# Kernel optimization log

Hardware: AMD Instinct MI355X
Metric: run time of the kernel (lower is better)

Reference implementation:

```python
import jax, jax.numpy as jnp
import numpy as np
import math

DIM = 1536; NH = 12; HD = 128
F, H, W = 6, 30, 30
S = F * H * W
B = 1
K_LEN = 9900  # hardcoded k_lens in the source forward
EPS_NORM = 1e-6


def _rope_tables(max_len=1024, d=HD):
    # Wan rope_params: three tables of widths d-4*(d//6), 2*(d//6), 2*(d//6)
    # -> cos/sin tables of half-widths 22, 21, 21 (concat = d//2 = 64)
    def ang(dd):
        inv = 1.0 / (10000.0 ** (np.arange(0, dd, 2, dtype=np.float64) / dd))
        return np.outer(np.arange(max_len, dtype=np.float64), inv)
    a = np.concatenate([ang(d - 4 * (d // 6)), ang(2 * (d // 6)), ang(2 * (d // 6))], axis=1)
    return np.cos(a).astype(np.float32), np.sin(a).astype(np.float32)


def setup_inputs() -> dict:
    key = jax.random.key(0)
    ks = jax.random.split(key, 5)
    s = 1.0 / math.sqrt(DIM)
    cos, sin = _rope_tables()
    return {
        "x": jax.random.normal(ks[0], (B, S, DIM), jnp.float32),
        "q_w": jax.random.normal(ks[1], (DIM, DIM), jnp.float32) * s,
        "q_b": jnp.zeros((DIM,), jnp.float32),
        "k_w": jax.random.normal(ks[2], (DIM, DIM), jnp.float32) * s,
        "k_b": jnp.zeros((DIM,), jnp.float32),
        "v_w": jax.random.normal(ks[3], (DIM, DIM), jnp.float32) * s,
        "v_b": jnp.zeros((DIM,), jnp.float32),
        "o_w": jax.random.normal(ks[4], (DIM, DIM), jnp.float32) * s,
        "o_b": jnp.zeros((DIM,), jnp.float32),
        "norm_q_w": jnp.ones((DIM,), jnp.float32),
        "norm_k_w": jnp.ones((DIM,), jnp.float32),
        "freqs_cos": jnp.asarray(cos),
        "freqs_sin": jnp.asarray(sin),
        "grid_f": F, "grid_h": H, "grid_w": W,
    }


def rms_norm(x, w):
    # RMSNorm over full model dim, computed in fp32 (as in source)
    xf = x.astype(jnp.float32)
    xn = xf * jax.lax.rsqrt(jnp.mean(xf * xf, axis=-1, keepdims=True) + EPS_NORM)
    return xn.astype(x.dtype) * w


def rope_apply(x, cos, sin, f, h, w):
    # x: [B,S,N,D]; rotate consecutive pairs with 3D-factorized (f,h,w) freqs
    Bb, Ss, Nn, Dd = x.shape
    c = Dd // 2
    sp = [c - 2 * (c // 3), c // 3, c // 3]  # 22, 21, 21

    def grid(tab):
        tf = tab[:, :sp[0]]
        th = tab[:, sp[0]:sp[0] + sp[1]]
        tw = tab[:, sp[0] + sp[1]:]
        g = jnp.concatenate([
            jnp.broadcast_to(tf[:f, None, None, :], (f, h, w, sp[0])),
            jnp.broadcast_to(th[None, :h, None, :], (f, h, w, sp[1])),
            jnp.broadcast_to(tw[None, None, :w, :], (f, h, w, sp[2])),
        ], axis=-1)
        return g.reshape(f * h * w, 1, c)  # [S,1,c] (broadcast over heads)

    gc, gs = grid(cos), grid(sin)
    xp = x.astype(jnp.float32).reshape(Bb, Ss, Nn, c, 2)
    xr, xi = xp[..., 0], xp[..., 1]
    orr = xr * gc - xi * gs
    oii = xr * gs + xi * gc
    return jnp.stack([orr, oii], axis=-1).reshape(Bb, Ss, Nn, Dd).astype(x.dtype)


def attention(q, k, v, k_len):
    # full attention (window_size=(-1,-1)) with keys masked beyond k_len
    scale = 1.0 / math.sqrt(q.shape[-1])
    att = jnp.einsum('bqnd,bknd->bnqk', q, k) * scale
    valid = jnp.arange(k.shape[1]) < k_len
    att = jnp.where(valid[None, None, None, :], att, jnp.finfo(att.dtype).min)
    p = jax.nn.softmax(att, axis=-1)
    return jnp.einsum('bnqk,bknd->bqnd', p, v)


def reference(x, q_w, q_b, k_w, k_b, v_w, v_b, o_w, o_b, norm_q_w, norm_k_w, freqs_cos, freqs_sin, grid_f, grid_h, grid_w):
    Bb, Ss, _ = x.shape
    q = rms_norm(x @ q_w.T + q_b, norm_q_w).reshape(Bb, Ss, NH, HD)
    k = rms_norm(x @ k_w.T + k_b, norm_k_w).reshape(Bb, Ss, NH, HD)
    v = (x @ v_w.T + v_b).reshape(Bb, Ss, NH, HD)
    q = rope_apply(q, freqs_cos, freqs_sin, grid_f, grid_h, grid_w)
    k = rope_apply(k, freqs_cos, freqs_sin, grid_f, grid_h, grid_w)
    o = attention(q, k, v, K_LEN).reshape(Bb, Ss, NH * HD)
    return o @ o_w.T + o_b
```

## Files before the change

kernel.cpp:

```cpp
#include <hip/hip_runtime.h>

#define DIM 1536
#define NH 12
#define HD 128
#define S_LEN 5400
#define SPAD 5440
#define MPAD 5504
#define NQKV 4608
#define EPS_NORM 1e-6f

typedef __bf16 bf16_t;
typedef __bf16 bf16x8 __attribute__((ext_vector_type(8)));
typedef __bf16 bf16x4 __attribute__((ext_vector_type(4)));
typedef float  f32x4  __attribute__((ext_vector_type(4)));

#define GLOAD_LDS16(gp, lp) __builtin_amdgcn_global_load_lds( \
    (__attribute__((address_space(1))) void*)(void*)(gp),     \
    (__attribute__((address_space(3))) void*)(lp), 16, 0, 0)


__global__ __launch_bounds__(256) void cvt_x_kernel(const float* __restrict__ x,
                                                    bf16_t* __restrict__ xb) {
  size_t base = ((size_t)blockIdx.x * 256 + threadIdx.x) * 4;
  if (base >= (size_t)MPAD * DIM) return;
  size_t row = base / DIM;
  float4 v = make_float4(0.f, 0.f, 0.f, 0.f);
  if (row < S_LEN) v = *(const float4*)&x[base];
  bf16x4 o; o[0] = (__bf16)v.x; o[1] = (__bf16)v.y; o[2] = (__bf16)v.z; o[3] = (__bf16)v.w;
  *(bf16x4*)&xb[base] = o;
}

__global__ __launch_bounds__(256) void cvt_wqkv_kernel(const float* __restrict__ qw,
                                                       const float* __restrict__ kw,
                                                       const float* __restrict__ vw,
                                                       bf16_t* __restrict__ wb) {
  size_t base = ((size_t)blockIdx.x * 256 + threadIdx.x) * 4;
  if (base >= (size_t)NQKV * DIM) return;
  int row = (int)(base / DIM);
  int col = (int)(base - (size_t)row * DIM);
  const float* src; int rr = row;
  if (rr >= 3072)      { src = vw; rr -= 3072; }
  else if (rr >= 1536) { src = kw; rr -= 1536; }
  else                 { src = qw; }
  float4 v = *(const float4*)&src[(size_t)rr * DIM + col];
  bf16x4 o; o[0] = (__bf16)v.x; o[1] = (__bf16)v.y; o[2] = (__bf16)v.z; o[3] = (__bf16)v.w;
  *(bf16x4*)&wb[base] = o;
}

__global__ __launch_bounds__(256) void cvt_wo_kernel(const float* __restrict__ w,
                                                     bf16_t* __restrict__ wb) {
  size_t base = ((size_t)blockIdx.x * 256 + threadIdx.x) * 4;
  if (base >= (size_t)DIM * DIM) return;
  float4 v = *(const float4*)&w[base];
  bf16x4 o; o[0] = (__bf16)v.x; o[1] = (__bf16)v.y; o[2] = (__bf16)v.z; o[3] = (__bf16)v.w;
  *(bf16x4*)&wb[base] = o;
}


template<bool OUT_BF16>
__global__ __launch_bounds__(256) void gemm_bt_kernel(
    const bf16_t* __restrict__ A, const bf16_t* __restrict__ B, void* __restrict__ C,
    const float* __restrict__ bias0, const float* __restrict__ bias1,
    const float* __restrict__ bias2, int M, int N, int K, int Mvalid) {
  __shared__ bf16_t As[128 * 32];
  __shared__ bf16_t Bs[128 * 32];
  int tid = threadIdx.x;
  int lane = tid & 63, wave = tid >> 6, quad = lane >> 4, l16 = lane & 15;
  int m0 = blockIdx.y * 128, n0 = blockIdx.x * 128;
  int wm = (wave >> 1) * 64, wn = (wave & 1) * 64;
  const bf16_t* Ab = A + (size_t)m0 * K;
  const bf16_t* Bb = B + (size_t)n0 * K;
  f32x4 acc[4][4] = {};
  for (int kt = 0; kt < K; kt += 32) {
    __syncthreads();
#pragma unroll
    for (int i = 0; i < 2; i++) {
      int eo = (i * 256 + tid) * 8;
      int row = eo >> 5, col = eo & 31;
      GLOAD_LDS16(Ab + (size_t)row * K + kt + col, &As[eo]);
      GLOAD_LDS16(Bb + (size_t)row * K + kt + col, &Bs[eo]);
    }
    __syncthreads();
    bf16x8 af[4], bfr[4];
#pragma unroll
    for (int i = 0; i < 4; i++)
      af[i] = *(const bf16x8*)&As[(wm + i * 16 + l16) * 32 + quad * 8];
#pragma unroll
    for (int j = 0; j < 4; j++)
      bfr[j] = *(const bf16x8*)&Bs[(wn + j * 16 + l16) * 32 + quad * 8];
#pragma unroll
    for (int i = 0; i < 4; i++)
#pragma unroll
      for (int j = 0; j < 4; j++)
        acc[i][j] = __builtin_amdgcn_mfma_f32_16x16x32_bf16(af[i], bfr[j], acc[i][j], 0, 0, 0);
  }
#pragma unroll
  for (int j = 0; j < 4; j++) {
    int n = n0 + wn + j * 16 + l16;
    float bias = (n < 1536) ? bias0[n] : (n < 3072) ? bias1[n - 1536] : bias2[n - 3072];
#pragma unroll
    for (int i = 0; i < 4; i++) {
#pragma unroll
      for (int r = 0; r < 4; r++) {
        int m = m0 + wm + i * 16 + quad * 4 + r;
        float v = acc[i][j][r] + bias;
        if (OUT_BF16) {
          ((bf16_t*)C)[(size_t)m * N + n] = (__bf16)v;
        } else {
          if (m < Mvalid) ((float*)C)[(size_t)m * N + n] = v;
        }
      }
    }
  }
}


__global__ __launch_bounds__(256) void rope_qk_kernel(
    const bf16_t* __restrict__ qkv, const float* __restrict__ nqw,
    const float* __restrict__ nkw, const float* __restrict__ fcos,
    const float* __restrict__ fsin, bf16_t* __restrict__ qout,
    bf16_t* __restrict__ kout) {
  int s = blockIdx.x;
  int tid = threadIdx.x;
  bool valid = s < S_LEN;
  int f = s / 900, hh = (s / 30) % 30, ww = s % 30;
  __shared__ float red[4];
  for (int which = 0; which < 2; which++) {
    const bf16_t* src = qkv + (size_t)s * NQKV + which * DIM;
    const float* nw = which ? nkw : nqw;
    bf16_t* dst = (which ? kout : qout) + (size_t)s * DIM;
    float osc = which ? 1.0f : 0.08838834764831845f;
    float v[6]; float ss = 0.f;
#pragma unroll
    for (int i = 0; i < 6; i++) {
      v[i] = valid ? (float)src[tid * 6 + i] : 0.f;
      ss += v[i] * v[i];
    }
#pragma unroll
    for (int off = 32; off >= 1; off >>= 1) ss += __shfl_down(ss, off);
    if ((tid & 63) == 0) red[tid >> 6] = ss;
    __syncthreads();
    float tot = red[0] + red[1] + red[2] + red[3];
    float rn = rsqrtf(tot * (1.f / DIM) + EPS_NORM);
    __syncthreads();
#pragma unroll
    for (int i = 0; i < 3; i++) {
      int e0 = tid * 6 + 2 * i;
      int p = e0 >> 1;
      int cc = p & 63;
      int pos = (cc < 22) ? f : (cc < 43) ? hh : ww;
      float c = fcos[pos * 64 + cc], sn = fsin[pos * 64 + cc];
      float xr = v[2 * i] * rn * nw[e0];
      float xi = v[2 * i + 1] * rn * nw[e0 + 1];
      dst[e0]     = (__bf16)((xr * c - xi * sn) * osc);
      dst[e0 + 1] = (__bf16)((xr * sn + xi * c) * osc);
    }
  }
}


__global__ __launch_bounds__(256) void v_transpose_kernel(const bf16_t* __restrict__ qkv,
                                                          bf16_t* __restrict__ vt) {
  __shared__ bf16_t tile[64][136];
  int h = blockIdx.y, s0 = blockIdx.x * 64, tid = threadIdx.x;
#pragma unroll
  for (int it = 0; it < 4; it++) {
    int eo = (it * 256 + tid) * 8;
    int row = eo >> 7, col = eo & 127;
    int s = s0 + row;
    bf16x8 val = {};
    if (s < S_LEN) val = *(const bf16x8*)&qkv[(size_t)s * NQKV + 3072 + h * HD + col];
    *(bf16x8*)&tile[row][col] = val;
  }
  __syncthreads();
  int d = tid & 127, j0 = (tid >> 7) * 32;
  bf16x8 outv[4];
#pragma unroll
  for (int b = 0; b < 4; b++)
#pragma unroll
    for (int j = 0; j < 8; j++) outv[b][j] = tile[j0 + b * 8 + j][d];
  size_t base = ((size_t)h * HD + d) * SPAD + s0 + j0;
#pragma unroll
  for (int b = 0; b < 4; b++) *(bf16x8*)&vt[base + b * 8] = outv[b];
}


__global__ __launch_bounds__(256, 2) void flash_attn_kernel(
    const bf16_t* __restrict__ q, const bf16_t* __restrict__ k,
    const bf16_t* __restrict__ vt, bf16_t* __restrict__ o) {
  __shared__ bf16_t Qs[128 * 128];
  __shared__ bf16_t Ks[64 * 128];
  __shared__ bf16_t Vs[128 * 64];
  __shared__ bf16_t PT[4][2][1024];
  int h = blockIdx.y;
  int s0 = blockIdx.x * 128;
  int tid = threadIdx.x, w = tid >> 6, lane = tid & 63;
  int quad = lane >> 4, l16 = lane & 15;

#pragma unroll
  for (int it = 0; it < 8; it++) {
    int slot = it * 256 + tid;
    int row = slot >> 4, pc = slot & 15;
    int c = (pc & 8) | ((pc & 7) ^ (row & 7));
    GLOAD_LDS16(q + (size_t)(s0 + row) * DIM + h * HD + c * 8, &Qs[slot * 8]);
  }
  __syncthreads();

  bf16x8 bq[2][4];
#pragma unroll
  for (int g = 0; g < 2; g++)
#pragma unroll
    for (int ks = 0; ks < 4; ks++) {
      int row = w * 32 + g * 16 + l16;
      int ch = ks * 4 + quad;
      int pc = (ch & 8) | ((ch & 7) ^ (l16 & 7));
      bq[g][ks] = *(const bf16x8*)&Qs[row * 128 + pc * 8];
    }

  float m_i[2] = {-1e30f, -1e30f}, l_i[2] = {0.f, 0.f};
  f32x4 oacc[2][8] = {};

  for (int kt = 0; kt < SPAD; kt += 64) {
    __syncthreads();
#pragma unroll
    for (int it = 0; it < 4; it++) {
      int slot = it * 256 + tid;
      int row = slot >> 4, pc = slot & 15;
      int c = (pc & 8) | ((pc & 7) ^ (row & 7));
      GLOAD_LDS16(k + (size_t)(kt + row) * DIM + h * HD + c * 8, &Ks[slot * 8]);
    }
#pragma unroll
    for (int it = 0; it < 4; it++) {
      int slot = it * 256 + tid;
      int d = slot >> 3, pc = slot & 7;
      int c = pc ^ (d & 7);
      GLOAD_LDS16(vt + ((size_t)h * HD + d) * SPAD + kt + c * 8, &Vs[slot * 8]);
    }
    __syncthreads();

    f32x4 sacc[2][4] = {};
#pragma unroll
    for (int ns = 0; ns < 4; ns++) {
      bf16x8 ak[4];
#pragma unroll
      for (int ks = 0; ks < 4; ks++) {
        int row = ns * 16 + l16;
        int ch = ks * 4 + quad;
        int pc = (ch & 8) | ((ch & 7) ^ (l16 & 7));
        ak[ks] = *(const bf16x8*)&Ks[row * 128 + pc * 8];
      }
#pragma unroll
      for (int g = 0; g < 2; g++)
#pragma unroll
        for (int ks = 0; ks < 4; ks++)
          sacc[g][ns] = __builtin_amdgcn_mfma_f32_16x16x32_bf16(ak[ks], bq[g][ks], sacc[g][ns], 0, 0, 0);
    }

    bool full = (kt + 64 <= S_LEN);
#pragma unroll
    for (int g = 0; g < 2; g++) {
      if (!full) {
#pragma unroll
        for (int ns = 0; ns < 4; ns++)
#pragma unroll
          for (int r = 0; r < 4; r++)
            if (kt + ns * 16 + quad * 4 + r >= S_LEN) sacc[g][ns][r] = -1e30f;
      }
      float mx = -1e30f;
#pragma unroll
      for (int ns = 0; ns < 4; ns++)
#pragma unroll
        for (int r = 0; r < 4; r++) mx = fmaxf(mx, sacc[g][ns][r]);
      mx = fmaxf(mx, __shfl_xor(mx, 16));
      mx = fmaxf(mx, __shfl_xor(mx, 32));
      float mn = fmaxf(m_i[g], mx);
      float al = __expf(m_i[g] - mn);
      m_i[g] = mn;
      float rs = 0.f;
#pragma unroll
      for (int ns = 0; ns < 4; ns++) {
        bf16x4 pk;
#pragma unroll
        for (int r = 0; r < 4; r++) {
          float p = __expf(sacc[g][ns][r] - mn);
          rs += p;
          pk[r] = (__bf16)p;
        }
        *(bf16x4*)&PT[w][g][(ns * 4 + quad) * 64 + l16 * 4] = pk;
      }
      rs += __shfl_xor(rs, 16);
      rs += __shfl_xor(rs, 32);
      l_i[g] = l_i[g] * al + rs;
#pragma unroll
      for (int dt = 0; dt < 8; dt++) oacc[g][dt] *= al;
    }

#pragma unroll
    for (int ks = 0; ks < 2; ks++) {
      bf16x8 bp[2];
#pragma unroll
      for (int g = 0; g < 2; g++) {
        bf16x4 lo = *(const bf16x4*)&PT[w][g][(ks * 8 + quad * 2) * 64 + l16 * 4];
        bf16x4 hi = *(const bf16x4*)&PT[w][g][(ks * 8 + quad * 2 + 1) * 64 + l16 * 4];
#pragma unroll
        for (int j = 0; j < 4; j++) { bp[g][j] = lo[j]; bp[g][j + 4] = hi[j]; }
      }
#pragma unroll
      for (int dt = 0; dt < 8; dt++) {
        int ch = ks * 4 + quad;
        int pc = ch ^ (l16 & 7);
        bf16x8 av = *(const bf16x8*)&Vs[(dt * 16 + l16) * 64 + pc * 8];
#pragma unroll
        for (int g = 0; g < 2; g++)
          oacc[g][dt] = __builtin_amdgcn_mfma_f32_16x16x32_bf16(av, bp[g], oacc[g][dt], 0, 0, 0);
      }
    }
  }

  bf16_t* Ot = Qs;
#pragma unroll
  for (int g = 0; g < 2; g++) {
    float inv = 1.f / l_i[g];
#pragma unroll
    for (int dt = 0; dt < 8; dt++) {
      bf16x4 v;
#pragma unroll
      for (int r = 0; r < 4; r++) v[r] = (__bf16)(oacc[g][dt][r] * inv);
      int qrow = w * 32 + g * 16 + l16;
      int c = dt * 2 + (quad >> 1);
      int pc = (c & 8) | ((c & 7) ^ (l16 & 7));
      *(bf16x4*)&Ot[qrow * 128 + pc * 8 + (quad & 1) * 4] = v;
    }
  }
  __syncthreads();
#pragma unroll
  for (int i = 0; i < 8; i++) {
    int q_ = i * 16 + (tid >> 4);
    int cc = tid & 15;
    int pc = (cc & 8) | ((cc & 7) ^ (q_ & 7));
    bf16x8 val = *(const bf16x8*)&Ot[q_ * 128 + pc * 8];
    int s = s0 + q_;
    if (s < S_LEN) *(bf16x8*)&o[(size_t)s * DIM + h * HD + cc * 8] = val;
  }
}


extern "C" void kernel_launch(void* const* d_in, const int* in_sizes, int n_in,
                              void* d_out, int out_size, void* d_ws, size_t ws_size,
                              hipStream_t stream) {
  const float* x    = (const float*)d_in[0];
  const float* q_w  = (const float*)d_in[1];
  const float* q_b  = (const float*)d_in[2];
  const float* k_w  = (const float*)d_in[3];
  const float* k_b  = (const float*)d_in[4];
  const float* v_w  = (const float*)d_in[5];
  const float* v_b  = (const float*)d_in[6];
  const float* o_w  = (const float*)d_in[7];
  const float* o_b  = (const float*)d_in[8];
  const float* nqw  = (const float*)d_in[9];
  const float* nkw  = (const float*)d_in[10];
  const float* fcos = (const float*)d_in[11];
  const float* fsin = (const float*)d_in[12];

  char* ws = (char*)d_ws;
  bf16_t* xb   = (bf16_t*)(ws + 0);
  bf16_t* wqkv = (bf16_t*)(ws + 16908288);
  bf16_t* wob  = (bf16_t*)(ws + 31064064);
  bf16_t* qkv  = (bf16_t*)(ws + 35782656);
  bf16_t* qb   = (bf16_t*)(ws + 86507520);
  bf16_t* kb   = (bf16_t*)(ws + 103415808);
  bf16_t* vtb  = (bf16_t*)(ws + 0);
  bf16_t* aob  = (bf16_t*)(ws + 35782656);

  cvt_x_kernel<<<(MPAD * DIM / 4 + 255) / 256, 256, 0, stream>>>(x, xb);
  cvt_wqkv_kernel<<<(NQKV * DIM / 4 + 255) / 256, 256, 0, stream>>>(q_w, k_w, v_w, wqkv);
  cvt_wo_kernel<<<(DIM * DIM / 4 + 255) / 256, 256, 0, stream>>>(o_w, wob);

  gemm_bt_kernel<true><<<dim3(NQKV / 128, MPAD / 128), 256, 0, stream>>>(
      xb, wqkv, qkv, q_b, k_b, v_b, MPAD, NQKV, DIM, MPAD);

  rope_qk_kernel<<<MPAD, 256, 0, stream>>>(qkv, nqw, nkw, fcos, fsin, qb, kb);
  v_transpose_kernel<<<dim3(SPAD / 64, NH), 256, 0, stream>>>(qkv, vtb);

  flash_attn_kernel<<<dim3(MPAD / 128, NH), 256, 0, stream>>>(qb, kb, vtb, aob);

  gemm_bt_kernel<false><<<dim3(DIM / 128, MPAD / 128), 256, 0, stream>>>(
      aob, wob, d_out, o_b, o_b, o_b, MPAD, DIM, DIM, S_LEN);
}
```

Before: 712.7 us.

## Shrink flash-attention LDS footprint to raise occupancy via register P shuffles

```diff
diff --git a/kernel.cpp b/kernel.cpp
--- a/kernel.cpp
+++ b/kernel.cpp
@@ -185,40 +185,31 @@
 }
 
 
-__global__ __launch_bounds__(256, 2) void flash_attn_kernel(
+__global__ __launch_bounds__(256, 3) void flash_attn_kernel(
     const bf16_t* __restrict__ q, const bf16_t* __restrict__ k,
     const bf16_t* __restrict__ vt, bf16_t* __restrict__ o) {
-  __shared__ bf16_t Qs[128 * 128];
-  __shared__ bf16_t Ks[64 * 128];
-  __shared__ bf16_t Vs[128 * 64];
-  __shared__ bf16_t PT[4][2][1024];
+  __shared__ bf16_t smem[16384];
+  bf16_t* Ks = smem;
+  bf16_t* Vs = smem + 8192;
   int h = blockIdx.y;
   int s0 = blockIdx.x * 128;
   int tid = threadIdx.x, w = tid >> 6, lane = tid & 63;
   int quad = lane >> 4, l16 = lane & 15;
 
-#pragma unroll
-  for (int it = 0; it < 8; it++) {
-    int slot = it * 256 + tid;
-    int row = slot >> 4, pc = slot & 15;
-    int c = (pc & 8) | ((pc & 7) ^ (row & 7));
-    GLOAD_LDS16(q + (size_t)(s0 + row) * DIM + h * HD + c * 8, &Qs[slot * 8]);
-  }
-  __syncthreads();
-
   bf16x8 bq[2][4];
 #pragma unroll
   for (int g = 0; g < 2; g++)
 #pragma unroll
     for (int ks = 0; ks < 4; ks++) {
-      int row = w * 32 + g * 16 + l16;
-      int ch = ks * 4 + quad;
-      int pc = (ch & 8) | ((ch & 7) ^ (l16 & 7));
-      bq[g][ks] = *(const bf16x8*)&Qs[row * 128 + pc * 8];
+      int qrow = s0 + w * 32 + g * 16 + l16;
+      bq[g][ks] = *(const bf16x8*)&q[(size_t)qrow * DIM + h * HD + ks * 32 + quad * 8];
     }
 
   float m_i[2] = {-1e30f, -1e30f}, l_i[2] = {0.f, 0.f};
   f32x4 oacc[2][8] = {};
+  int sA = (quad & 1) * 32 + l16;
+  int sB = sA + 16;
+  bool selhi = quad >= 2;
 
   for (int kt = 0; kt < SPAD; kt += 64) {
     __syncthreads();
@@ -257,6 +248,7 @@
     }
 
     bool full = (kt + 64 <= S_LEN);
+    unsigned int pkl[2][4], pkh[2][4];
 #pragma unroll
     for (int g = 0; g < 2; g++) {
       if (!full) {
@@ -286,7 +278,8 @@
           rs += p;
           pk[r] = (__bf16)p;
         }
-        *(bf16x4*)&PT[w][g][(ns * 4 + quad) * 64 + l16 * 4] = pk;
+        union { bf16x4 v; unsigned int u[2]; } cv; cv.v = pk;
+        pkl[g][ns] = cv.u[0]; pkh[g][ns] = cv.u[1];
       }
       rs += __shfl_xor(rs, 16);
       rs += __shfl_xor(rs, 32);
@@ -300,10 +293,20 @@
       bf16x8 bp[2];
 #pragma unroll
       for (int g = 0; g < 2; g++) {
-        bf16x4 lo = *(const bf16x4*)&PT[w][g][(ks * 8 + quad * 2) * 64 + l16 * 4];
-        bf16x4 hi = *(const bf16x4*)&PT[w][g][(ks * 8 + quad * 2 + 1) * 64 + l16 * 4];
-#pragma unroll
-        for (int j = 0; j < 4; j++) { bp[g][j] = lo[j]; bp[g][j + 4] = hi[j]; }
+        int b0 = __shfl((int)pkl[g][2 * ks], sA);
+        int b1 = __shfl((int)pkh[g][2 * ks], sA);
+        int b2 = __shfl((int)pkl[g][2 * ks], sB);
+        int b3 = __shfl((int)pkh[g][2 * ks], sB);
+        int c0 = __shfl((int)pkl[g][2 * ks + 1], sA);
+        int c1 = __shfl((int)pkh[g][2 * ks + 1], sA);
+        int c2 = __shfl((int)pkl[g][2 * ks + 1], sB);
+        int c3 = __shfl((int)pkh[g][2 * ks + 1], sB);
+        union { unsigned int u[4]; bf16x8 v; } cv;
+        cv.u[0] = selhi ? (unsigned)c0 : (unsigned)b0;
+        cv.u[1] = selhi ? (unsigned)c1 : (unsigned)b1;
+        cv.u[2] = selhi ? (unsigned)c2 : (unsigned)b2;
+        cv.u[3] = selhi ? (unsigned)c3 : (unsigned)b3;
+        bp[g] = cv.v;
       }
 #pragma unroll
       for (int dt = 0; dt < 8; dt++) {
@@ -317,7 +320,8 @@
     }
   }
 
-  bf16_t* Ot = Qs;
+  __syncthreads();
+  bf16_t* Ot = smem;
 #pragma unroll
   for (int g = 0; g < 2; g++) {
     float inv = 1.f / l_i[g];
```

Result: slower. 742.8 us (+4.2%).

## Switch flash attention to 32x32x16 MFMA tiles with register-resident Q

Applied to the files above, without the earlier changes.

```diff
diff --git a/kernel.cpp b/kernel.cpp
--- a/kernel.cpp
+++ b/kernel.cpp
@@ -13,6 +13,7 @@
 typedef __bf16 bf16x8 __attribute__((ext_vector_type(8)));
 typedef __bf16 bf16x4 __attribute__((ext_vector_type(4)));
 typedef float  f32x4  __attribute__((ext_vector_type(4)));
+typedef float  f32x16 __attribute__((ext_vector_type(16)));
 
 #define GLOAD_LDS16(gp, lp) __builtin_amdgcn_global_load_lds( \
     (__attribute__((address_space(1))) void*)(void*)(gp),     \
@@ -188,37 +189,23 @@
 __global__ __launch_bounds__(256, 2) void flash_attn_kernel(
     const bf16_t* __restrict__ q, const bf16_t* __restrict__ k,
     const bf16_t* __restrict__ vt, bf16_t* __restrict__ o) {
-  __shared__ bf16_t Qs[128 * 128];
   __shared__ bf16_t Ks[64 * 128];
-  __shared__ bf16_t Vs[128 * 64];
-  __shared__ bf16_t PT[4][2][1024];
-  int h = blockIdx.y;
+  __shared__ bf16_t Vs[64 * 128];
+  __shared__ bf16_t Pw[4][32 * 64];
+  int head = blockIdx.y;
   int s0 = blockIdx.x * 128;
   int tid = threadIdx.x, w = tid >> 6, lane = tid & 63;
-  int quad = lane >> 4, l16 = lane & 15;
-
-#pragma unroll
-  for (int it = 0; it < 8; it++) {
-    int slot = it * 256 + tid;
-    int row = slot >> 4, pc = slot & 15;
-    int c = (pc & 8) | ((pc & 7) ^ (row & 7));
-    GLOAD_LDS16(q + (size_t)(s0 + row) * DIM + h * HD + c * 8, &Qs[slot * 8]);
-  }
-  __syncthreads();
-
-  bf16x8 bq[2][4];
-#pragma unroll
-  for (int g = 0; g < 2; g++)
-#pragma unroll
-    for (int ks = 0; ks < 4; ks++) {
-      int row = w * 32 + g * 16 + l16;
-      int ch = ks * 4 + quad;
-      int pc = (ch & 8) | ((ch & 7) ^ (l16 & 7));
-      bq[g][ks] = *(const bf16x8*)&Qs[row * 128 + pc * 8];
-    }
-
-  float m_i[2] = {-1e30f, -1e30f}, l_i[2] = {0.f, 0.f};
-  f32x4 oacc[2][8] = {};
+  int l31 = lane & 31, hh = lane >> 5;
+
+  bf16x8 bq[8];
+  {
+    const bf16_t* qp = &q[(size_t)(s0 + w * 32 + l31) * DIM + head * HD + hh * 8];
+#pragma unroll
+    for (int kc = 0; kc < 8; kc++) bq[kc] = *(const bf16x8*)(qp + kc * 16);
+  }
+
+  float m_i = -1e30f, l_i = 0.f;
+  f32x16 oacc[4] = {};
 
   for (int kt = 0; kt < SPAD; kt += 64) {
     __syncthreads();
@@ -226,121 +213,128 @@
     for (int it = 0; it < 4; it++) {
       int slot = it * 256 + tid;
       int row = slot >> 4, pc = slot & 15;
-      int c = (pc & 8) | ((pc & 7) ^ (row & 7));
-      GLOAD_LDS16(k + (size_t)(kt + row) * DIM + h * HD + c * 8, &Ks[slot * 8]);
+      int c = pc ^ (row & 15);
+      GLOAD_LDS16(k + (size_t)(kt + row) * DIM + head * HD + c * 8, &Ks[slot * 8]);
     }
 #pragma unroll
     for (int it = 0; it < 4; it++) {
       int slot = it * 256 + tid;
-      int d = slot >> 3, pc = slot & 7;
-      int c = pc ^ (d & 7);
-      GLOAD_LDS16(vt + ((size_t)h * HD + d) * SPAD + kt + c * 8, &Vs[slot * 8]);
-    }
-    __syncthreads();
-
-    f32x4 sacc[2][4] = {};
-#pragma unroll
-    for (int ns = 0; ns < 4; ns++) {
-      bf16x8 ak[4];
-#pragma unroll
-      for (int ks = 0; ks < 4; ks++) {
-        int row = ns * 16 + l16;
-        int ch = ks * 4 + quad;
-        int pc = (ch & 8) | ((ch & 7) ^ (l16 & 7));
-        ak[ks] = *(const bf16x8*)&Ks[row * 128 + pc * 8];
-      }
-#pragma unroll
-      for (int g = 0; g < 2; g++)
-#pragma unroll
-        for (int ks = 0; ks < 4; ks++)
-          sacc[g][ns] = __builtin_amdgcn_mfma_f32_16x16x32_bf16(ak[ks], bq[g][ks], sacc[g][ns], 0, 0, 0);
-    }
-
-    bool full = (kt + 64 <= S_LEN);
-#pragma unroll
-    for (int g = 0; g < 2; g++) {
-      if (!full) {
-#pragma unroll
-        for (int ns = 0; ns < 4; ns++)
-#pragma unroll
-          for (int r = 0; r < 4; r++)
-            if (kt + ns * 16 + quad * 4 + r >= S_LEN) sacc[g][ns][r] = -1e30f;
-      }
-      float mx = -1e30f;
-#pragma unroll
-      for (int ns = 0; ns < 4; ns++)
-#pragma unroll
-        for (int r = 0; r < 4; r++) mx = fmaxf(mx, sacc[g][ns][r]);
-      mx = fmaxf(mx, __shfl_xor(mx, 16));
-      mx = fmaxf(mx, __shfl_xor(mx, 32));
-      float mn = fmaxf(m_i[g], mx);
-      float al = __expf(m_i[g] - mn);
-      m_i[g] = mn;
-      float rs = 0.f;
-#pragma unroll
-      for (int ns = 0; ns < 4; ns++) {
+      int row = slot >> 4, pc = slot & 15;
+      int cp = pc ^ (row & 15);
+      int d = 2 * row + (cp >> 3);
+      GLOAD_LDS16(vt + ((size_t)head * HD + d) * SPAD + kt + (cp & 7) * 8, &Vs[slot * 8]);
+    }
+    __syncthreads();
+
+    f32x16 sacc[2] = {};
+#pragma unroll
+    for (int ns = 0; ns < 2; ns++) {
+      int row = ns * 32 + l31;
+#pragma unroll
+      for (int kc = 0; kc < 8; kc++) {
+        int pc = (kc * 2 + hh) ^ (row & 15);
+        bf16x8 ak = *(const bf16x8*)&Ks[row * 128 + pc * 8];
+        sacc[ns] = __builtin_amdgcn_mfma_f32_32x32x16_bf16(ak, bq[kc], sacc[ns], 0, 0, 0);
+      }
+    }
+
+    if (kt + 64 > S_LEN) {
+#pragma unroll
+      for (int ns = 0; ns < 2; ns++)
+#pragma unroll
+        for (int r = 0; r < 16; r++) {
+          int kvg = kt + ns * 32 + (r & 3) + 8 * (r >> 2) + 4 * hh;
+          if (kvg >= S_LEN) sacc[ns][r] = -1e30f;
+        }
+    }
+
+    float mx = -1e30f;
+#pragma unroll
+    for (int ns = 0; ns < 2; ns++)
+#pragma unroll
+      for (int r = 0; r < 16; r++) mx = fmaxf(mx, sacc[ns][r]);
+    mx = fmaxf(mx, __shfl_xor(mx, 32));
+    float mn = fmaxf(m_i, mx);
+    float al = __expf(m_i - mn);
+    m_i = mn;
+    float rs = 0.f;
+#pragma unroll
+    for (int ns = 0; ns < 2; ns++)
+#pragma unroll
+      for (int r = 0; r < 16; r++) {
+        float p = __expf(sacc[ns][r] - mn);
+        rs += p;
+        sacc[ns][r] = p;
+      }
+    rs += __shfl_xor(rs, 32);
+    l_i = l_i * al + rs;
+#pragma unroll
+    for (int dt = 0; dt < 4; dt++)
+#pragma unroll
+      for (int r = 0; r < 16; r++) oacc[dt][r] *= al;
+
+#pragma unroll
+    for (int ns = 0; ns < 2; ns++)
+#pragma unroll
+      for (int t = 0; t < 4; t++) {
         bf16x4 pk;
 #pragma unroll
-        for (int r = 0; r < 4; r++) {
-          float p = __expf(sacc[g][ns][r] - mn);
-          rs += p;
-          pk[r] = (__bf16)p;
-        }
-        *(bf16x4*)&PT[w][g][(ns * 4 + quad) * 64 + l16 * 4] = pk;
-      }
-      rs += __shfl_xor(rs, 16);
-      rs += __shfl_xor(rs, 32);
-      l_i[g] = l_i[g] * al + rs;
-#pragma unroll
-      for (int dt = 0; dt < 8; dt++) oacc[g][dt] *= al;
-    }
-
-#pragma unroll
-    for (int ks = 0; ks < 2; ks++) {
-      bf16x8 bp[2];
-#pragma unroll
-      for (int g = 0; g < 2; g++) {
-        bf16x4 lo = *(const bf16x4*)&PT[w][g][(ks * 8 + quad * 2) * 64 + l16 * 4];
-        bf16x4 hi = *(const bf16x4*)&PT[w][g][(ks * 8 + quad * 2 + 1) * 64 + l16 * 4];
-#pragma unroll
-        for (int j = 0; j < 4; j++) { bp[g][j] = lo[j]; bp[g][j + 4] = hi[j]; }
-      }
-#pragma unroll
-      for (int dt = 0; dt < 8; dt++) {
-        int ch = ks * 4 + quad;
-        int pc = ch ^ (l16 & 7);
-        bf16x8 av = *(const bf16x8*)&Vs[(dt * 16 + l16) * 64 + pc * 8];
-#pragma unroll
-        for (int g = 0; g < 2; g++)
-          oacc[g][dt] = __builtin_amdgcn_mfma_f32_16x16x32_bf16(av, bp[g], oacc[g][dt], 0, 0, 0);
-      }
-    }
-  }
-
-  bf16_t* Ot = Qs;
-#pragma unroll
-  for (int g = 0; g < 2; g++) {
-    float inv = 1.f / l_i[g];
-#pragma unroll
-    for (int dt = 0; dt < 8; dt++) {
-      bf16x4 v;
-#pragma unroll
-      for (int r = 0; r < 4; r++) v[r] = (__bf16)(oacc[g][dt][r] * inv);
-      int qrow = w * 32 + g * 16 + l16;
-      int c = dt * 2 + (quad >> 1);
-      int pc = (c & 8) | ((c & 7) ^ (l16 & 7));
-      *(bf16x4*)&Ot[qrow * 128 + pc * 8 + (quad & 1) * 4] = v;
-    }
-  }
-  __syncthreads();
-#pragma unroll
-  for (int i = 0; i < 8; i++) {
-    int q_ = i * 16 + (tid >> 4);
-    int cc = tid & 15;
-    int pc = (cc & 8) | ((cc & 7) ^ (q_ & 7));
-    bf16x8 val = *(const bf16x8*)&Ot[q_ * 128 + pc * 8];
-    int s = s0 + q_;
-    if (s < S_LEN) *(bf16x8*)&o[(size_t)s * DIM + h * HD + cc * 8] = val;
+        for (int r4 = 0; r4 < 4; r4++) pk[r4] = (__bf16)sacc[ns][t * 4 + r4];
+        int c8 = ns * 8 + 2 * t + hh;
+        int pc8 = c8 ^ (l31 & 15);
+        *(bf16x4*)&Pw[w][l31 * 64 + pc8 * 4] = pk;
+      }
+
+#pragma unroll
+    for (int kvc = 0; kvc < 4; kvc++) {
+      int c8a = kvc * 4 + hh * 2;
+      bf16x4 plo = *(const bf16x4*)&Pw[w][l31 * 64 + ((c8a) ^ (l31 & 15)) * 4];
+      bf16x4 phi = *(const bf16x4*)&Pw[w][l31 * 64 + ((c8a + 1) ^ (l31 & 15)) * 4];
+      bf16x8 bp;
+#pragma unroll
+      for (int j = 0; j < 4; j++) { bp[j] = plo[j]; bp[j + 4] = phi[j]; }
+#pragma unroll
+      for (int dt = 0; dt < 4; dt++) {
+        int d = dt * 32 + l31;
+        int r = d >> 1;
+        int cp = ((d & 1) << 3) | (kvc * 2 + hh);
+        int pc = cp ^ (r & 15);
+        bf16x8 av = *(const bf16x8*)&Vs[r * 128 + pc * 8];
+        oacc[dt] = __builtin_amdgcn_mfma_f32_32x32x16_bf16(av, bp, oacc[dt], 0, 0, 0);
+      }
+    }
+  }
+
+  float inv = 1.f / l_i;
+  int qr = lane >> 1, seg = lane & 1;
+  int srow = s0 + w * 32 + qr;
+#pragma unroll
+  for (int half = 0; half < 2; half++) {
+#pragma unroll
+    for (int dl = 0; dl < 2; dl++) {
+      int dt = half * 2 + dl;
+#pragma unroll
+      for (int t = 0; t < 4; t++) {
+        bf16x4 v;
+#pragma unroll
+        for (int r4 = 0; r4 < 4; r4++) v[r4] = (__bf16)(oacc[dt][t * 4 + r4] * inv);
+        int c8 = dl * 8 + 2 * t + hh;
+        int pc8 = c8 ^ (l31 & 15);
+        *(bf16x4*)&Pw[w][l31 * 64 + pc8 * 4] = v;
+      }
+    }
+#pragma unroll
+    for (int i = 0; i < 4; i++) {
+      int c8 = seg * 8 + 2 * i;
+      bf16x4 lo = *(const bf16x4*)&Pw[w][qr * 64 + ((c8) ^ (qr & 15)) * 4];
+      bf16x4 hi = *(const bf16x4*)&Pw[w][qr * 64 + ((c8 + 1) ^ (qr & 15)) * 4];
+      bf16x8 val;
+#pragma unroll
+      for (int j = 0; j < 4; j++) { val[j] = lo[j]; val[j + 4] = hi[j]; }
+      if (srow < S_LEN)
+        *(bf16x8*)&o[(size_t)srow * DIM + head * HD + half * 64 + seg * 32 + i * 8] = val;
+    }
+    __syncthreads();
   }
 }
 
```

Result: faster. 692.0 us (-2.9%).
